# Optimization experiments

Measured on AMD Instinct MI355X. Metric: run time of the kernel, lower is better.

Reference implementation:

```python
import jax, jax.numpy as jnp
from jax import lax
import numpy as np

GAMMA = 1.0
BIG = 1e10  # stands in for +inf; exp(-BIG/gamma) == 0 in fp32, safe under autodiff


def cosine_distance_matrix(x, y):
    # x: [B,N,d], y: [B,M,d] -> D: [B,N,M] = 1 - cos(x_i, y_j)
    xn = x / (jnp.linalg.norm(x, axis=-1, keepdims=True) + 1e-8)
    yn = y / (jnp.linalg.norm(y, axis=-1, keepdims=True) + 1e-8)
    return 1.0 - jnp.einsum('bnd,bmd->bnm', xn, yn)


def soft_dtw(D, gamma):
    # D: [B,N,M]. Returns R[:, N, M] of the soft-DTW DP:
    # R[i,j] = D[i-1,j-1] + softmin(R[i-1,j-1], R[i-1,j], R[i,j-1])
    B, N, M = D.shape
    # column j=0: R[:,0,0]=0, R[:,i,0]=inf for i>=1  -> shape [B, N+1]
    init_col = jnp.concatenate([jnp.zeros((B, 1), D.dtype),
                                jnp.full((B, N), BIG, D.dtype)], axis=1)

    def col_step(prev_col, d_col):
        # prev_col: R[:, 0:N+1, j-1]  [B, N+1];  d_col: D[:, :, j-1]  [B, N]
        def row_step(carry, inp):
            r_diag, r_up, d = inp  # each [B]: R[i-1,j-1], R[i-1,j]... (see below)
            stacked = jnp.stack([r_diag, carry, r_up], axis=0)  # [3,B]
            softmin = -gamma * jax.nn.logsumexp(-stacked / gamma, axis=0)
            r = d + softmin
            return r, r
        # per-row inputs along i=1..N: diag=prev_col[i-1], up-in-column=prev_col[i]
        inputs = (prev_col[:, :-1].T, prev_col[:, 1:].T, d_col.T)  # each [N,B]
        _, rows = lax.scan(row_step, jnp.full((B,), BIG, D.dtype), inputs)
        new_col = jnp.concatenate([jnp.full((B, 1), BIG, D.dtype), rows.T], axis=1)
        return new_col, None

    final_col, _ = lax.scan(col_step, init_col, jnp.transpose(D, (2, 0, 1)))
    return final_col[:, -1]  # R[:, N, M]


def setup_inputs() -> dict:
    key = jax.random.key(0)
    k1, k2 = jax.random.split(key)
    B, N, M, d = 16, 1024, 1024, 128
    x = jax.random.normal(k1, (B, N, d), dtype=jnp.float32)
    y = jax.random.normal(k2, (B, M, d), dtype=jnp.float32)
    return {"x": x, "y": y}


def reference(x, y):
    D = cosine_distance_matrix(x, y)
    return soft_dtw(D, GAMMA)  # [B]
```

## Files before the change

### kernel.cpp

```cpp
#include <hip/hip_runtime.h>
#include <hip/hip_fp16.h>

#define BATCH 16
#define NROW 1024
#define MCOL 1024
#define DFEAT 128

#define R_DP 4
#define C_DP 8
#define NCH (MCOL / C_DP)
#define NPHT 384
#define BATCH_BYTES 2097152

#define L2E 1.4426950408889634f
#define LN2 0.6931471805599453f

typedef __attribute__((ext_vector_type(8))) short short8;
typedef __attribute__((ext_vector_type(4))) float f32x4;

__device__ inline unsigned short f2bf(float f) {
  unsigned u = __float_as_uint(f);
  return (unsigned short)((u + 0x7fff + ((u >> 16) & 1)) >> 16);
}

__device__ __forceinline__ int pbase(int P) {
  return (P < 128) ? 32 * P * (P + 1)
       : (P < 256) ? 528384 + ((P - 128) << 13)
                   : 1576960 + 32 * (16256 - (383 - P) * (384 - P));
}

__global__ __launch_bounds__(256) void norm_kernel(
    const float* __restrict__ x, const float* __restrict__ y,
    unsigned short* __restrict__ xnb, unsigned short* __restrict__ ynb) {
  int row = blockIdx.x * 4 + (threadIdx.x >> 6);
  int lane = threadIdx.x & 63;
  const float* src;
  unsigned short* dst;
  if (row < BATCH * NROW) {
    src = x + (size_t)row * DFEAT;
    dst = xnb + (size_t)row * DFEAT;
  } else {
    int r2 = row - BATCH * NROW;
    src = y + (size_t)r2 * DFEAT;
    dst = ynb + (size_t)r2 * DFEAT;
  }
  float2 v = *(const float2*)(src + lane * 2);
  float s = v.x * v.x + v.y * v.y;
  #pragma unroll
  for (int o = 32; o > 0; o >>= 1) s += __shfl_xor(s, o, 64);
  float inv = 1.0f / (sqrtf(s) + 1e-8f);
  unsigned short b0 = f2bf(v.x * inv), b1 = f2bf(v.y * inv);
  *(unsigned*)(dst + lane * 2) = (unsigned)b0 | ((unsigned)b1 << 16);
}

__global__ __launch_bounds__(256) void dist_kernel(
    const unsigned short* __restrict__ xnb, const unsigned short* __restrict__ ynb,
    char* __restrict__ Dpar) {
  __shared__ __align__(16) unsigned char xsb[128 * 256];
  __shared__ __align__(16) unsigned char ysb[128 * 256];

  int b = blockIdx.z, ti0 = blockIdx.y, tj0 = blockIdx.x;
  int I0 = ti0 * 128, J0 = tj0 * 128;
  int tid = threadIdx.x;

  const uint4* xsrc = (const uint4*)(xnb + (size_t)(b * NROW + I0) * DFEAT);
  const uint4* ysrc = (const uint4*)(ynb + (size_t)(b * MCOL + J0) * DFEAT);
  #pragma unroll
  for (int it = 0; it < 8; ++it) {
    int idx = tid + it * 256;
    int row = idx >> 4, cb = (idx & 15) * 16;
    int swz = row * 256 + (cb ^ ((row & 7) << 4));
    *(uint4*)&xsb[swz] = xsrc[idx];
    *(uint4*)&ysb[swz] = ysrc[idx];
  }
  __syncthreads();

  int wid = tid >> 6, lane = tid & 63;
  int wi = wid >> 1, wj = wid & 1;
  int lr = lane & 15, lk = lane >> 4;

  f32x4 acc[4][4] = {};
  #pragma unroll
  for (int ks = 0; ks < 4; ++ks) {
    int cb = ks * 64 + lk * 16;
    short8 af[4], bf[4];
    #pragma unroll
    for (int ti = 0; ti < 4; ++ti) {
      int row = wi * 64 + ti * 16 + lr;
      af[ti] = *(short8*)&xsb[row * 256 + (cb ^ ((row & 7) << 4))];
    }
    #pragma unroll
    for (int tj = 0; tj < 4; ++tj) {
      int row = wj * 64 + tj * 16 + lr;
      bf[tj] = *(short8*)&ysb[row * 256 + (cb ^ ((row & 7) << 4))];
    }
    #pragma unroll
    for (int ti = 0; ti < 4; ++ti)
      #pragma unroll
      for (int tj = 0; tj < 4; ++tj)
        acc[ti][tj] = __builtin_amdgcn_mfma_f32_16x16x32_bf16(
            af[ti], bf[tj], acc[ti][tj], 0, 0, 0);
  }

  char* Db = Dpar + (size_t)b * BATCH_BYTES;
  #pragma unroll
  for (int ti = 0; ti < 4; ++ti) {
    int gi0 = I0 + wi * 64 + ti * 16 + lk * 4;
    int gl = gi0 >> 2;
    #pragma unroll
    for (int tj = 0; tj < 4; ++tj) {
      int gj = J0 + wj * 64 + tj * 16 + lr;
      int c = gj >> 3, k = gj & 7;
      int P = c + gl;
      int gmn = P > 127 ? P - 127 : 0;
      char* slot = Db + pbase(P) + ((gl - gmn) << 6) + (k << 1);
      #pragma unroll
      for (int v = 0; v < 4; ++v) {
        float d = 1.0f - acc[ti][tj][v];
        *(__half*)(slot + v * 16) = __float2half(exp2f(-d * L2E));
      }
    }
  }
}


#define MIXMUL_LO(A, h, s) \
  asm("v_fma_mix_f32 %0, %1, %2, %3 op_sel_hi:[1,0,0]" : "=v"(A) : "v"(h), "v"(s), "v"(fzero))
#define MIXMUL_HI(A, h, s) \
  asm("v_fma_mix_f32 %0, %1, %2, %3 op_sel:[1,0,0] op_sel_hi:[1,0,0]" : "=v"(A) : "v"(h), "v"(s), "v"(fzero))
#define MIXFMA_LO(lf, h, a) \
  asm("v_fma_mix_f32 %0, %1, %2, %3 op_sel_hi:[1,0,0]" : "=v"(lf) : "v"(h), "v"(lf), "v"(a))
#define MIXFMA_HI(lf, h, a) \
  asm("v_fma_mix_f32 %0, %1, %2, %3 op_sel:[1,0,0] op_sel_hi:[1,0,0]" : "=v"(lf) : "v"(h), "v"(lf), "v"(a))

__device__ __forceinline__ float shup(float x, bool edge) {
  int xi = __float_as_int(x);
  int sh = __builtin_amdgcn_update_dpp(xi, xi, 0x111, 0xF, 0xF, false);
  int bc = __builtin_amdgcn_update_dpp(xi, xi, 0x142, 0xF, 0xF, false);
  return __int_as_float(edge ? bc : sh);
}

__device__ __forceinline__ void dtw_phase4(int cbase, int t, int w, bool edge,
    const uint4* L, float* carry, float (&B)[9], float& O, float fzero,
    const float* bndPrev) {
  int c = cbase - t;
  float U[9];
  #pragma unroll
  for (int k = 0; k < 9; ++k) U[k] = shup(B[k], edge);
  float Oin = shup(O, edge);
  if (t == 0) {
    if (w == 0) {
      #pragma unroll
      for (int k = 0; k < 9; ++k) U[k] = 0.0f;
      U[0] = (c == 0) ? 1.0f : 0.0f;
      Oin = O;
    } else {
      #pragma unroll
      for (int k = 0; k < 9; ++k) U[k] = bndPrev[k];
      Oin = bndPrev[9];
    }
  }
  if ((unsigned)c < 128u) {
    if (c == 0) O = Oin;
    float sc = exp2f((O - Oin) * L2E);
    #pragma unroll
    for (int k = 0; k < 9; ++k) U[k] *= sc;

    #pragma unroll
    for (int r = 0; r < R_DP; ++r) {
      uint4 d = L[r];
      unsigned dw[4] = {d.x, d.y, d.z, d.w};
      float S[8], A[8];
      #pragma unroll
      for (int k = 0; k < 8; ++k) S[k] = U[k] + U[k + 1];
      #pragma unroll
      for (int q = 0; q < 4; ++q) {
        MIXMUL_LO(A[2 * q],     dw[q], S[2 * q]);
        MIXMUL_HI(A[2 * q + 1], dw[q], S[2 * q + 1]);
      }
      float oldc = carry[r], lf = oldc;
      float V[8];
      #pragma unroll
      for (int q = 0; q < 4; ++q) {
        MIXFMA_LO(lf, dw[q], A[2 * q]);     V[2 * q] = lf;
        MIXFMA_HI(lf, dw[q], A[2 * q + 1]); V[2 * q + 1] = lf;
      }
      U[0] = oldc;
      #pragma unroll
      for (int k = 1; k <= 8; ++k) U[k] = V[k - 1];
      carry[r] = lf;
    }

    float rep = carry[R_DP - 1];
    int ex = (int)((__float_as_uint(rep) >> 23) & 0xFF) - 127;
    if ((ex < -20 || ex > 12) && ex < 128) {
      float s = __uint_as_float((unsigned)(127 - ex) << 23);
      #pragma unroll
      for (int r = 0; r < R_DP; ++r) carry[r] *= s;
      #pragma unroll
      for (int k = 0; k < 9; ++k) U[k] *= s;
      O -= (float)ex * LN2;
    }
    #pragma unroll
    for (int k = 0; k < 9; ++k) B[k] = U[k];
  }
}

#define GL4(Lr, SB, OFF) \
  asm volatile("global_load_dwordx4 %0, %1, %2 offset:" OFF : "=v"(Lr) : "v"(voff), "s"(SB));
#define ISSUE4(L, SB) \
  GL4(L[0], SB, "0") GL4(L[1], SB, "16") GL4(L[2], SB, "32") GL4(L[3], SB, "48")

#define STEP(P, CUR, NXT)                                                    \
  {                                                                          \
    int Pn = (P) + 1;                                                        \
    int gmn = Pn > 127 ? Pn - 127 : 0;                                       \
    const char* sb = gb + (pbase(Pn) + ((w64 - gmn) << 6));                  \
    ISSUE4(NXT, sb)                                                          \
    asm volatile("s_waitcnt vmcnt(4)" ::: "memory");                         \
    __builtin_amdgcn_sched_barrier(0);                                       \
    if ((unsigned)((P) - w64) < 191u) {                                      \
      dtw_phase4((P) - w64, t, w, edge, CUR, carry, B, O, fzero,             \
                 &bnd[(P) & 1][w > 0 ? w - 1 : 0][0]);                       \
      if (t == 63) {                                                         \
        float* bn = &bnd[((P) + 1) & 1][w][0];                               \
        _Pragma("unroll")                                                    \
        for (int k = 0; k < 9; ++k) bn[k] = B[k];                            \
        bn[9] = O;                                                           \
      }                                                                      \
    }                                                                        \
    asm volatile("s_waitcnt lgkmcnt(0)" ::: "memory");                       \
    __builtin_amdgcn_s_barrier();                                            \
    asm volatile("" ::: "memory");                                           \
  }

__global__ __launch_bounds__(256, 1) void dtw_kernel(
    const char* __restrict__ Dpar, float* __restrict__ out) {
  int b = blockIdx.x;
  int tid = threadIdx.x;
  int w = __builtin_amdgcn_readfirstlane(tid >> 6);
  int t = tid & 63;
  int w64 = w << 6;
  const bool edge = (t != 0) && ((t & 15) == 0);
  float fzero = 0.0f;
  int voff = t << 6;

  __shared__ float bnd[2][4][10];
  if (tid < 80) ((float*)bnd)[tid] = 0.0f;
  __syncthreads();

  const char* gb = Dpar + (size_t)b * BATCH_BYTES;

  float carry[R_DP] = {0.f, 0.f, 0.f, 0.f};
  float B[9] = {};
  float O = 0.0f;

  uint4 LA[R_DP], LB[R_DP];
  {
    const char* sb = gb + (w64 << 6);
    ISSUE4(LA, sb)
  }

  for (int p = 0; p < NPHT; p += 2) {
    STEP(p, LA, LB)
    STEP(p + 1, LB, LA)
  }

  asm volatile("s_waitcnt vmcnt(0)" ::: "memory");

  if (tid == 255) out[b] = O - logf(carry[R_DP - 1]);
}

extern "C" void kernel_launch(void* const* d_in, const int* in_sizes, int n_in,
                              void* d_out, int out_size, void* d_ws, size_t ws_size,
                              hipStream_t stream) {
  const float* x = (const float*)d_in[0];
  const float* y = (const float*)d_in[1];
  float* out = (float*)d_out;

  char* ws = (char*)d_ws;
  char* Dpar = ws;
  size_t dp_bytes = (size_t)BATCH * BATCH_BYTES;
  unsigned short* xnb = (unsigned short*)(ws + dp_bytes);
  unsigned short* ynb = xnb + (size_t)BATCH * NROW * DFEAT;

  norm_kernel<<<(2 * BATCH * NROW) / 4, 256, 0, stream>>>(x, y, xnb, ynb);
  dist_kernel<<<dim3(MCOL / 128, NROW / 128, BATCH), 256, 0, stream>>>(
      xnb, ynb, Dpar);
  dtw_kernel<<<BATCH, 256, 0, stream>>>(Dpar, out);
}
```

Measured before the change: 292.5 us.

## Switch soft-DTW wavefront to 8 rows per lane with two waves

Each lane of the DP kernel now handles 8 rows instead of 4, so the block shrinks to 128 threads (2 waves) and the number of anti-diagonal phases drops from 384 to 255. The D-matrix layout written by the distance kernel is changed to match the new 8-row-per-lane wavefront ordering, and the load schedule issues eight loads per phase with per-wave issue windows. The intent is to cut the count of serial phases and block barriers on the critical path, at the cost of more per-lane serial work and register pressure per phase. The renormalisation step also gains a guard so it only runs when the carried value is positive.

```diff
diff --git a/kernel.cpp b/kernel.cpp
--- a/kernel.cpp
+++ b/kernel.cpp
@@ -6,10 +6,10 @@
 #define MCOL 1024
 #define DFEAT 128
 
-#define R_DP 4
+#define R_DP 8
 #define C_DP 8
 #define NCH (MCOL / C_DP)
-#define NPHT 384
+#define NPH2 255
 #define BATCH_BYTES 2097152
 
 #define L2E 1.4426950408889634f
@@ -23,10 +23,11 @@
   return (unsigned short)((u + 0x7fff + ((u >> 16) & 1)) >> 16);
 }
 
-__device__ __forceinline__ int pbase(int P) {
-  return (P < 128) ? 32 * P * (P + 1)
-       : (P < 256) ? 528384 + ((P - 128) << 13)
-                   : 1576960 + 32 * (16256 - (383 - P) * (384 - P));
+__device__ __forceinline__ int wphase(int p) { return p < 128 ? p + 1 : 255 - p; }
+__device__ __forceinline__ int l2minf(int p) { return p > 127 ? p - 127 : 0; }
+__device__ __forceinline__ int sbase(int p) {
+  return p <= 128 ? 64 * p * (p + 1)
+                  : BATCH_BYTES - 64 * (255 - p) * (256 - p);
 }
 
 __global__ __launch_bounds__(256) void norm_kernel(
@@ -55,7 +56,7 @@
 
 __global__ __launch_bounds__(256) void dist_kernel(
     const unsigned short* __restrict__ xnb, const unsigned short* __restrict__ ynb,
-    char* __restrict__ Dpar) {
+    char* __restrict__ Dc) {
   __shared__ __align__(16) unsigned char xsb[128 * 256];
   __shared__ __align__(16) unsigned char ysb[128 * 256];
 
@@ -102,22 +103,23 @@
             af[ti], bf[tj], acc[ti][tj], 0, 0, 0);
   }
 
-  char* Db = Dpar + (size_t)b * BATCH_BYTES;
+  char* Db = Dc + (size_t)b * BATCH_BYTES;
   #pragma unroll
   for (int ti = 0; ti < 4; ++ti) {
     int gi0 = I0 + wi * 64 + ti * 16 + lk * 4;
-    int gl = gi0 >> 2;
+    int l2 = gi0 >> 3, r2b = gi0 & 7;
     #pragma unroll
     for (int tj = 0; tj < 4; ++tj) {
       int gj = J0 + wj * 64 + tj * 16 + lr;
       int c = gj >> 3, k = gj & 7;
-      int P = c + gl;
-      int gmn = P > 127 ? P - 127 : 0;
-      char* slot = Db + pbase(P) + ((gl - gmn) << 6) + (k << 1);
+      int p = c + l2;
+      int wv = wphase(p), l2m = l2minf(p);
+      char* slot = Db + sbase(p) + r2b * (wv << 4) + ((l2 - l2m) << 4) + (k << 1);
+      int rs = wv << 4;
       #pragma unroll
       for (int v = 0; v < 4; ++v) {
         float d = 1.0f - acc[ti][tj][v];
-        *(__half*)(slot + v * 16) = __float2half(exp2f(-d * L2E));
+        *(__half*)(slot + v * rs) = __float2half(exp2f(-d * L2E));
       }
     }
   }
@@ -140,16 +142,15 @@
   return __int_as_float(edge ? bc : sh);
 }
 
-__device__ __forceinline__ void dtw_phase4(int cbase, int t, int w, bool edge,
+__device__ __forceinline__ void dtw_phase8(int c, int t, bool isw0, bool edge,
     const uint4* L, float* carry, float (&B)[9], float& O, float fzero,
     const float* bndPrev) {
-  int c = cbase - t;
   float U[9];
   #pragma unroll
   for (int k = 0; k < 9; ++k) U[k] = shup(B[k], edge);
   float Oin = shup(O, edge);
   if (t == 0) {
-    if (w == 0) {
+    if (isw0) {
       #pragma unroll
       for (int k = 0; k < 9; ++k) U[k] = 0.0f;
       U[0] = (c == 0) ? 1.0f : 0.0f;
@@ -192,83 +193,96 @@
     }
 
     float rep = carry[R_DP - 1];
-    int ex = (int)((__float_as_uint(rep) >> 23) & 0xFF) - 127;
-    if ((ex < -20 || ex > 12) && ex < 128) {
-      float s = __uint_as_float((unsigned)(127 - ex) << 23);
-      #pragma unroll
-      for (int r = 0; r < R_DP; ++r) carry[r] *= s;
-      #pragma unroll
-      for (int k = 0; k < 9; ++k) U[k] *= s;
-      O -= (float)ex * LN2;
+    if (rep > 0.0f) {
+      int ex = (int)((__float_as_uint(rep) >> 23) & 0xFF) - 127;
+      if ((ex < -20 || ex > 12) && ex < 128) {
+        float s = __uint_as_float((unsigned)(127 - ex) << 23);
+        #pragma unroll
+        for (int r = 0; r < R_DP; ++r) carry[r] *= s;
+        #pragma unroll
+        for (int k = 0; k < 9; ++k) U[k] *= s;
+        O -= (float)ex * LN2;
+      }
     }
     #pragma unroll
     for (int k = 0; k < 9; ++k) B[k] = U[k];
   }
 }
 
-#define GL4(Lr, SB, OFF) \
-  asm volatile("global_load_dwordx4 %0, %1, %2 offset:" OFF : "=v"(Lr) : "v"(voff), "s"(SB));
-#define ISSUE4(L, SB) \
-  GL4(L[0], SB, "0") GL4(L[1], SB, "16") GL4(L[2], SB, "32") GL4(L[3], SB, "48")
-
-#define STEP(P, CUR, NXT)                                                    \
-  {                                                                          \
-    int Pn = (P) + 1;                                                        \
-    int gmn = Pn > 127 ? Pn - 127 : 0;                                       \
-    const char* sb = gb + (pbase(Pn) + ((w64 - gmn) << 6));                  \
-    ISSUE4(NXT, sb)                                                          \
-    asm volatile("s_waitcnt vmcnt(4)" ::: "memory");                         \
-    __builtin_amdgcn_sched_barrier(0);                                       \
-    if ((unsigned)((P) - w64) < 191u) {                                      \
-      dtw_phase4((P) - w64, t, w, edge, CUR, carry, B, O, fzero,             \
-                 &bnd[(P) & 1][w > 0 ? w - 1 : 0][0]);                       \
-      if (t == 63) {                                                         \
-        float* bn = &bnd[((P) + 1) & 1][w][0];                               \
-        _Pragma("unroll")                                                    \
-        for (int k = 0; k < 9; ++k) bn[k] = B[k];                            \
-        bn[9] = O;                                                           \
-      }                                                                      \
-    }                                                                        \
-    asm volatile("s_waitcnt lgkmcnt(0)" ::: "memory");                       \
-    __builtin_amdgcn_s_barrier();                                            \
-    asm volatile("" ::: "memory");                                           \
-  }
-
-__global__ __launch_bounds__(256, 1) void dtw_kernel(
-    const char* __restrict__ Dpar, float* __restrict__ out) {
+#define GLP(Lr, SB) \
+  asm volatile("global_load_dwordx4 %0, %1, %2" : "=v"(Lr) : "v"(voff), "s"(SB));
+
+#define ISSUE8()                                                 \
+  GLP(L[0], sb0) GLP(L[1], sb1) GLP(L[2], sb2) GLP(L[3], sb3)    \
+  GLP(L[4], sb4) GLP(L[5], sb5) GLP(L[6], sb6) GLP(L[7], sb7)
+
+__global__ __launch_bounds__(128, 1) void dtw_kernel(
+    const char* __restrict__ Dc, float* __restrict__ out) {
+  __shared__ float bnd[2][10];
   int b = blockIdx.x;
   int tid = threadIdx.x;
   int w = __builtin_amdgcn_readfirstlane(tid >> 6);
   int t = tid & 63;
-  int w64 = w << 6;
+  int l2 = (w << 6) + t;
   const bool edge = (t != 0) && ((t & 15) == 0);
   float fzero = 0.0f;
-  int voff = t << 6;
-
-  __shared__ float bnd[2][4][10];
-  if (tid < 80) ((float*)bnd)[tid] = 0.0f;
+  int vbase = l2 << 4;
+
+  if (tid < 20) ((float*)bnd)[tid] = 0.0f;
   __syncthreads();
 
-  const char* gb = Dpar + (size_t)b * BATCH_BYTES;
-
-  float carry[R_DP] = {0.f, 0.f, 0.f, 0.f};
+  const char* g = Dc + (size_t)b * BATCH_BYTES;
+
+  float carry[R_DP];
+  #pragma unroll
+  for (int r = 0; r < R_DP; ++r) carry[r] = 0.0f;
   float B[9] = {};
   float O = 0.0f;
-
-  uint4 LA[R_DP], LB[R_DP];
-  {
-    const char* sb = gb + (w64 << 6);
-    ISSUE4(LA, sb)
-  }
-
-  for (int p = 0; p < NPHT; p += 2) {
-    STEP(p, LA, LB)
-    STEP(p + 1, LB, LA)
+  uint4 L[R_DP];
+
+  if (w == 0) {
+    const char* sb0 = g,       * sb1 = g + 16,  * sb2 = g + 32,  * sb3 = g + 48;
+    const char* sb4 = g + 64,  * sb5 = g + 80,  * sb6 = g + 96,  * sb7 = g + 112;
+    int voff = vbase;
+    if ((unsigned)(0 - l2) < 128u) { ISSUE8() }
+  }
+
+  for (int P = 0; P < NPH2 - 1; ++P) {
+    int pn = P + 1;
+    int wv = wphase(pn), l2m = l2minf(pn);
+    const char* gS = g + sbase(pn);
+    int rs = wv << 4;
+    const char* sb0 = gS,          * sb1 = gS + rs,     * sb2 = gS + 2 * rs;
+    const char* sb3 = gS + 3 * rs, * sb4 = gS + 4 * rs, * sb5 = gS + 5 * rs;
+    const char* sb6 = gS + 6 * rs, * sb7 = gS + 7 * rs;
+    int voff = vbase - (l2m << 4);
+    bool doissue = (w == 0) ? (pn <= 190) : (pn >= 64);
+    if (doissue) {
+      if ((unsigned)(pn - l2) < 128u) { ISSUE8() }
+      asm volatile("s_waitcnt vmcnt(8)" ::: "memory");
+    } else {
+      asm volatile("s_waitcnt vmcnt(0)" ::: "memory");
+    }
+    __builtin_amdgcn_sched_barrier(0);
+
+    dtw_phase8(P - l2, t, w == 0, edge, L, carry, B, O, fzero, &bnd[P & 1][0]);
+
+    if (w == 0 && t == 63) {
+      #pragma unroll
+      for (int k = 0; k < 9; ++k) bnd[(P + 1) & 1][k] = B[k];
+      bnd[(P + 1) & 1][9] = O;
+    }
+    asm volatile("s_waitcnt lgkmcnt(0)" ::: "memory");
+    __builtin_amdgcn_s_barrier();
+    asm volatile("" ::: "memory");
   }
 
   asm volatile("s_waitcnt vmcnt(0)" ::: "memory");
-
-  if (tid == 255) out[b] = O - logf(carry[R_DP - 1]);
+  __builtin_amdgcn_sched_barrier(0);
+  dtw_phase8(254 - l2, t, w == 0, edge, L, carry, B, O, fzero,
+             &bnd[254 & 1][0]);
+
+  if (w == 1 && t == 63) out[b] = O - logf(carry[R_DP - 1]);
 }
 
 extern "C" void kernel_launch(void* const* d_in, const int* in_sizes, int n_in,
@@ -279,13 +293,13 @@
   float* out = (float*)d_out;
 
   char* ws = (char*)d_ws;
-  char* Dpar = ws;
+  char* Dc = ws;
   size_t dp_bytes = (size_t)BATCH * BATCH_BYTES;
   unsigned short* xnb = (unsigned short*)(ws + dp_bytes);
   unsigned short* ynb = xnb + (size_t)BATCH * NROW * DFEAT;
 
   norm_kernel<<<(2 * BATCH * NROW) / 4, 256, 0, stream>>>(x, y, xnb, ynb);
   dist_kernel<<<dim3(MCOL / 128, NROW / 128, BATCH), 256, 0, stream>>>(
-      xnb, ynb, Dpar);
-  dtw_kernel<<<BATCH, 256, 0, stream>>>(Dpar, out);
-}
+      xnb, ynb, Dc);
+  dtw_kernel<<<BATCH, 128, 0, stream>>>(Dc, out);
+}
```

New measurement: 298.1 us. Within noise of the previous version (+1.9%).
